# Kernel tuning notes

Hardware: AMD Instinct MI355X
Metric: run time of the kernel (lower is better)

Reference implementation:

```python
import jax, jax.numpy as jnp
import numpy as np

B, T, V, E, L, H = 128, 512, 128, 64, 128, 512  # batch, seq, vocab, char_emb, latent, hidden


def setup_inputs() -> dict:
    key = jax.random.key(0)
    ks = jax.random.split(key, 12)
    r = lambda k, shape, s=0.05: jax.random.normal(k, shape, dtype=jnp.float32) * s
    return {
        "char_ids": jax.random.randint(ks[0], (B, T), 0, V),
        "z": jax.random.normal(ks[1], (B, L), dtype=jnp.float32),
        "emb": r(ks[2], (V, E)),
        "cw1": r(ks[3], (L, H)), "cb1": jnp.zeros((H,)), "cg1": jnp.ones((H,)), "cbeta1": jnp.zeros((H,)),
        "cw2": r(ks[4], (H, H)), "cb2": jnp.zeros((H,)), "cg2": jnp.ones((H,)), "cbeta2": jnp.zeros((H,)),
        "wih0": r(ks[5], (4 * H, E + H + 2)), "whh0": r(ks[6], (4 * H, H)),
        "bih0": jnp.zeros((4 * H,)), "bhh0": jnp.zeros((4 * H,)),
        "wih1": r(ks[7], (4 * H, H)), "whh1": r(ks[8], (4 * H, H)),
        "bih1": jnp.zeros((4 * H,)), "bhh1": jnp.zeros((4 * H,)),
        "wo1": r(ks[9], (H, H // 2)), "bo1": jnp.zeros((H // 2,)),
        "wo2": r(ks[10], (H // 2, 2)), "bo2": jnp.zeros((2,)),
        "init_timing": jnp.zeros((2,)),
    }


def _ln(x, g, b, eps=1e-5):
    m = jnp.mean(x, -1, keepdims=True)
    v = jnp.var(x, -1, keepdims=True)
    return (x - m) * jax.lax.rsqrt(v + eps) * g + b


def _lstm_cell(x, h, c, wih, whh, bih, bhh):
    # PyTorch gate order: i, f, g, o
    gates = x @ wih.T + bih + h @ whh.T + bhh
    i, f, g, o = jnp.split(gates, 4, axis=-1)
    c = jax.nn.sigmoid(f) * c + jax.nn.sigmoid(i) * jnp.tanh(g)
    h = jax.nn.sigmoid(o) * jnp.tanh(c)
    return h, c


def reference(char_ids, z, emb, cw1, cb1, cg1, cbeta1, cw2, cb2, cg2, cbeta2,
              wih0, whh0, bih0, bhh0, wih1, whh1, bih1, bhh1,
              wo1, bo1, wo2, bo2, init_timing):
    b = char_ids.shape[0]
    # condition encoder: Linear -> LN -> LeakyReLU(0.2), twice
    cond = jax.nn.leaky_relu(_ln(z @ cw1 + cb1, cg1, cbeta1), 0.2)
    cond = jax.nn.leaky_relu(_ln(cond @ cw2 + cb2, cg2, cbeta2), 0.2)  # (B, H)
    xs = jnp.transpose(emb[char_ids], (1, 0, 2))  # (T, B, E)
    h0 = jnp.zeros((b, H), jnp.float32)
    c0 = jnp.zeros((b, H), jnp.float32)
    h1 = jnp.zeros((b, H), jnp.float32)
    c1 = jnp.zeros((b, H), jnp.float32)
    prev = jnp.broadcast_to(init_timing, (b, 2))

    def step(carry, xt):
        h0, c0, h1, c1, prev = carry
        xin = jnp.concatenate([xt, cond, prev], axis=-1)  # (B, E+H+2)
        h0, c0 = _lstm_cell(xin, h0, c0, wih0, whh0, bih0, bhh0)
        h1, c1 = _lstm_cell(h0, h1, c1, wih1, whh1, bih1, bhh1)
        out = jax.nn.leaky_relu(h1 @ wo1 + bo1, 0.2) @ wo2 + bo2
        out = jax.nn.softplus(out) + 0.005  # (B, 2)
        return (h0, c0, h1, c1, out), out

    _, ys = jax.lax.scan(step, (h0, c0, h1, c1, prev), xs)
    return jnp.transpose(ys, (1, 0, 2))  # (B, T, 2)
```

## Files before the change

kernel.cpp:

```cpp
#include <hip/hip_runtime.h>

#define Bn 128
#define Tn 512
#define Vn 128
#define En 64
#define Ln 128
#define Hn 512
#define G4 2048
#define WGS 256
#define NTHR 512
#define NALL (WGS * NTHR)
#define LSTR 520
#define GRPS 8
#define WPG 32
#define RPG 16

typedef unsigned short u16;
typedef unsigned int u32;
typedef __bf16 bf16x8 __attribute__((ext_vector_type(8)));
typedef float f32x4 __attribute__((ext_vector_type(4)));
typedef u32 u32x4 __attribute__((ext_vector_type(4)));

__device__ inline float bf2f(u16 h) {
    u32 u = ((u32)h) << 16;
    float f;
    __builtin_memcpy(&f, &u, 4);
    return f;
}
__device__ inline u16 f2bf(float f) {
    u32 u;
    __builtin_memcpy(&u, &f, 4);
    u32 r = (u + 0x7fffu + ((u >> 16) & 1u)) >> 16;
    return (u16)r;
}
__device__ inline u32 f2u(float f) { u32 u; __builtin_memcpy(&u, &f, 4); return u; }
__device__ inline float u2f(u32 u) { float f; __builtin_memcpy(&f, &u, 4); return f; }
__device__ inline float sigm(float x) { return 1.f / (1.f + expf(-x)); }
__device__ inline float leaky(float x) { return x > 0.f ? x : 0.2f * x; }
__device__ inline float softplus(float x) {
    return x > 0.f ? x + log1pf(expf(-x)) : log1pf(expf(x));
}

__device__ inline void cload16(const u32* p, u32* w) {
    u32x4 v0, v1, v2, v3;
    asm volatile(
        "global_load_dwordx4 %0, %4, off sc0 sc1\n\t"
        "global_load_dwordx4 %1, %4, off offset:16 sc0 sc1\n\t"
        "global_load_dwordx4 %2, %4, off offset:32 sc0 sc1\n\t"
        "global_load_dwordx4 %3, %4, off offset:48 sc0 sc1\n\t"
        "s_waitcnt vmcnt(0)"
        : "=&v"(v0), "=&v"(v1), "=&v"(v2), "=&v"(v3)
        : "v"(p)
        : "memory");
    *(u32x4*)(w) = v0;
    *(u32x4*)(w + 4) = v1;
    *(u32x4*)(w + 8) = v2;
    *(u32x4*)(w + 12) = v3;
}
__device__ inline u32 cload1(const u32* p) {
    u32 v;
    asm volatile("global_load_dword %0, %1, off sc0 sc1\n\ts_waitcnt vmcnt(0)"
                 : "=v"(v) : "v"(p) : "memory");
    return v;
}
__device__ inline void cwait() { asm volatile("s_waitcnt vmcnt(0)" ::: "memory"); }
__device__ inline void cstore1(u32* p, u32 v) {
    asm volatile("global_store_dword %0, %1, off sc0 sc1" :: "v"(p), "v"(v) : "memory");
}

#define OFF_FLAGS  0x000000
#define OFF_B1SUM  0x002000
#define OFF_WP     0x004000
#define OFF_BIAS0  0x008000
#define OFF_CPAR   0x00A000
#define OFF_H0P    0x010000
#define OFF_H1P    0x050000
#define OFF_PART   0x090000
#define OFF_WO1TH  0x0B0000
#define OFF_WO1TL  0x0F0000
#define OFF_ZF     0x130000
#define OFF_CW1F   0x140000
#define OFF_CW2F   0x180000
#define OFF_CONDF  0x280000
#define OFF_YBUF   0x2C0000
#define OFF_BASE0  0x300000
#define OFF_EMBW   0x400000
#define OFF_W0HI   0x500000
#define OFF_W0LO   0x700000
#define OFF_W1HI   0x900000
#define OFF_W1LO   0xB00000
#define OFF_WI1HI  0xD00000
#define OFF_WI1LO  0xF00000

__device__ inline void gbar_heavy(int* cnt, int* gen) {
    __syncthreads();
    if (threadIdx.x == 0) {
        __threadfence();
        int g = __hip_atomic_load(gen, __ATOMIC_RELAXED, __HIP_MEMORY_SCOPE_AGENT);
        int arrived = __hip_atomic_fetch_add(cnt, 1, __ATOMIC_ACQ_REL, __HIP_MEMORY_SCOPE_AGENT);
        if (arrived == WGS - 1) {
            __hip_atomic_store(cnt, 0, __ATOMIC_RELAXED, __HIP_MEMORY_SCOPE_AGENT);
            __hip_atomic_store(gen, g + 1, __ATOMIC_RELEASE, __HIP_MEMORY_SCOPE_AGENT);
        } else {
            while (__hip_atomic_load(gen, __ATOMIC_ACQUIRE, __HIP_MEMORY_SCOPE_AGENT) == g)
                __builtin_amdgcn_s_sleep(1);
        }
        __threadfence();
    }
    __syncthreads();
}

__device__ inline void poll32(const u32* gf, u32 sq) {
    const int l = threadIdx.x & 31;
    for (;;) {
        u32 v = cload1(gf + l);
        if (__all((int)(v >= sq))) break;
        __builtin_amdgcn_s_sleep(4);
    }
}
__device__ inline void poll16(const u32* gf, u32 sq) {
    const int l = threadIdx.x & 15;
    for (;;) {
        u32 v = cload1(gf + l);
        if (__all((int)(v >= sq))) break;
        __builtin_amdgcn_s_sleep(4);
    }
}

__device__ inline void unpack16(const u32* w, u16* ph, u16* pl) {
    u32 hd[8], ld[8];
#pragma unroll
    for (int i = 0; i < 8; ++i) {
        hd[i] = (w[2 * i] & 0xFFFFu) | (w[2 * i + 1] << 16);
        ld[i] = (w[2 * i] >> 16) | (w[2 * i + 1] & 0xFFFF0000u);
    }
    *(u32x4*)(ph) = *(const u32x4*)(hd);
    *(u32x4*)(ph + 8) = *(const u32x4*)(hd + 4);
    *(u32x4*)(pl) = *(const u32x4*)(ld);
    *(u32x4*)(pl + 8) = *(const u32x4*)(ld + 4);
}

#define MF(a, b, c) __builtin_amdgcn_mfma_f32_16x16x32_bf16(a, b, c, 0, 0, 0)

__device__ inline f32x4 gemm16_3(const u16* __restrict__ Ah, const u16* __restrict__ Al,
                                 const u16* __restrict__ Bhb, const u16* __restrict__ Blb,
                                 int colb, int n, int q) {
    const u16* Bh = Bhb + (size_t)(colb + n) * Hn;
    const u16* Bl = Blb + (size_t)(colb + n) * Hn;
    const int a0 = n * LSTR;
    f32x4 c0 = {0.f, 0.f, 0.f, 0.f}, c1 = c0, c2 = c0;
#pragma unroll 4
    for (int it = 0; it < 16; ++it) {
        const int ko = it * 32 + q * 8;
        bf16x8 bh = *(const bf16x8*)(Bh + ko);
        bf16x8 bl = *(const bf16x8*)(Bl + ko);
        bf16x8 ah = *(const bf16x8*)(Ah + a0 + ko);
        bf16x8 al = *(const bf16x8*)(Al + a0 + ko);
        c0 = MF(ah, bh, c0);
        c1 = MF(al, bh, c1);
        c2 = MF(ah, bl, c2);
    }
    return c0 + c1 + c2;
}

__device__ inline f32x4 gemm16_regB3(const u16* __restrict__ Ah, const u16* __restrict__ Al,
                                     const bf16x8* wa, const bf16x8* wb, int n, int q) {
    const int a0 = n * LSTR;
    f32x4 c0 = {0.f, 0.f, 0.f, 0.f}, c1 = c0, c2 = c0;
#pragma unroll
    for (int it = 0; it < 16; ++it) {
        const int ko = it * 32 + q * 8;
        bf16x8 ah = *(const bf16x8*)(Ah + a0 + ko);
        bf16x8 al = *(const bf16x8*)(Al + a0 + ko);
        c0 = MF(ah, wa[it], c0);
        c1 = MF(al, wa[it], c1);
        c2 = MF(ah, wb[it], c2);
    }
    return c0 + c1 + c2;
}

__device__ inline f32x4 gemm16_regB2(const u16* __restrict__ Ah, const u16* __restrict__ Al,
                                     const bf16x8* wb, int n, int q) {
    const int a0 = n * LSTR;
    f32x4 c0 = {0.f, 0.f, 0.f, 0.f}, c1 = c0;
#pragma unroll
    for (int it = 0; it < 16; ++it) {
        const int ko = it * 32 + q * 8;
        bf16x8 ah = *(const bf16x8*)(Ah + a0 + ko);
        bf16x8 al = *(const bf16x8*)(Al + a0 + ko);
        c0 = MF(ah, wb[it], c0);
        c1 = MF(al, wb[it], c1);
    }
    return c0 + c1;
}

__device__ inline f32x4 gemm16_ldsB3(const u16* __restrict__ Ah, const u16* __restrict__ Al,
                                     const u16* __restrict__ Bh, const u16* __restrict__ Bl,
                                     int n, int q) {
    const int a0 = n * LSTR;
    f32x4 c0 = {0.f, 0.f, 0.f, 0.f}, c1 = c0, c2 = c0;
#pragma unroll 4
    for (int it = 0; it < 16; ++it) {
        const int ko = it * 32 + q * 8;
        bf16x8 bh = *(const bf16x8*)(Bh + a0 + ko);
        bf16x8 bl = *(const bf16x8*)(Bl + a0 + ko);
        bf16x8 ah = *(const bf16x8*)(Ah + a0 + ko);
        bf16x8 al = *(const bf16x8*)(Al + a0 + ko);
        c0 = MF(ah, bh, c0);
        c1 = MF(al, bh, c1);
        c2 = MF(ah, bl, c2);
    }
    return c0 + c1 + c2;
}

__device__ inline void stage(float* dst, const void* src, int n, int gtid, bool isbf) {
    if (isbf) {
        const u16* s = (const u16*)src;
// ... 54 lines not shown
        e2 += ldw<ISBF>(emb, (size_t)(bb0 + 64) * En + k) * w;
        e3 += ldw<ISBF>(emb, (size_t)(bb0 + 96) * En + k) * w;
    }
    embW[(size_t)bb0 * G4 + cc] = e0;
    embW[(size_t)(bb0 + 32) * G4 + cc] = e1;
    embW[(size_t)(bb0 + 64) * G4 + cc] = e2;
    embW[(size_t)(bb0 + 96) * G4 + cc] = e3;
}

__device__ inline void ln_leaky_row(const float* __restrict__ x, const float* __restrict__ gamma,
                                    const float* __restrict__ beta, float* __restrict__ out,
                                    float* red) {
    int tid = threadIdx.x;
    float v = x[tid];
    float s = v, s2 = v * v;
    for (int off = 32; off; off >>= 1) {
        s += __shfl_down(s, off);
        s2 += __shfl_down(s2, off);
    }
    int wv = tid >> 6;
    if ((tid & 63) == 0) { red[wv * 2] = s; red[wv * 2 + 1] = s2; }
    __syncthreads();
    if (tid == 0) {
        float ts = 0.f, ts2 = 0.f;
        for (int i = 0; i < 8; ++i) { ts += red[i * 2]; ts2 += red[i * 2 + 1]; }
        float m = ts / 512.f;
        float var = ts2 / 512.f - m * m;
        red[16] = m;
        red[17] = rsqrtf(var + 1e-5f);
    }
    __syncthreads();
    float m = red[16], rs = red[17];
    out[tid] = leaky((v - m) * rs * gamma[tid] + beta[tid]);
    __syncthreads();
}

__global__ void init_flags_kernel(int* flags) { flags[threadIdx.x] = 0; }

__global__ __launch_bounds__(NTHR, 2) void gen_kernel(
    const int* __restrict__ char_ids, const void* z, const void* emb,
    const void* cw1, const void* cb1, const void* cg1, const void* cbeta1,
    const void* cw2, const void* cb2, const void* cg2, const void* cbeta2,
    const void* wih0, const void* whh0, const void* bih0, const void* bhh0,
    const void* wih1, const void* whh1, const void* bih1, const void* bhh1,
    const void* wo1, const void* bo1, const void* wo2, const void* bo2,
    const void* init_t, void* outp, char* __restrict__ ws) {
    __shared__ u16 lh0h[RPG * LSTR];
    __shared__ u16 lh0l[RPG * LSTR];
    __shared__ u16 lh1h[RPG * LSTR];
    __shared__ u16 lh1l[RPG * LSTR];
    __shared__ u16 lwoh[16 * LSTR];
    __shared__ u16 lwol[16 * LSTR];
    __shared__ float smemx[1024];
    __shared__ float pvs[32];
    __shared__ float red[34];

    int* flags = (int*)(ws + OFF_FLAGS);
    float* b1sum = (float*)(ws + OFF_B1SUM);
    float* wpb = (float*)(ws + OFF_WP);
    float* bias0f = (float*)(ws + OFF_BIAS0);
    float* cpar = (float*)(ws + OFF_CPAR);
    u32* h0p = (u32*)(ws + OFF_H0P);
    u32* h1p = (u32*)(ws + OFF_H1P);
    float* partf = (float*)(ws + OFF_PART);
    u16* wo1Th = (u16*)(ws + OFF_WO1TH);
    u16* wo1Tl = (u16*)(ws + OFF_WO1TL);
    float* zf = (float*)(ws + OFF_ZF);
    float* cw1f = (float*)(ws + OFF_CW1F);
    float* cw2f = (float*)(ws + OFF_CW2F);
    float* condf = (float*)(ws + OFF_CONDF);
    float* ybuf = (float*)(ws + OFF_YBUF);
    float* base0 = (float*)(ws + OFF_BASE0);
    float* embW = (float*)(ws + OFF_EMBW);
    u16* W0hi = (u16*)(ws + OFF_W0HI);
    u16* W0lo = (u16*)(ws + OFF_W0LO);
    u16* W1hi = (u16*)(ws + OFF_W1HI);
    u16* W1lo = (u16*)(ws + OFF_W1LO);
    u16* Wi1hi = (u16*)(ws + OFF_WI1HI);
    u16* Wi1lo = (u16*)(ws + OFF_WI1LO);
    float* wo1f = base0;

    const bool isbf = (((const u32*)cg1)[0] == 0x3F803F80u);

    const int g = blockIdx.x;
    const int tid = threadIdx.x;
    const int wv = tid >> 6;
    const int grp = g >> 5;
    const int ut = g & 31;
    const int mat = wv >> 2;
    const int gw = wv & 3;
    const int R0g = grp * RPG;
    const int colb = gw * 512 + ut * 16;
    const int lane = tid & 63;
    const int n = lane & 15;
    const int q = lane >> 4;
    const int gtid = g * NTHR + tid;
    const f32x4 Z4 = {0.f, 0.f, 0.f, 0.f};

    u32* gf = (u32*)flags + grp * 64;
    u32* gf2 = (u32*)flags + grp * 64 + 32;
    u32* gfl = gf + ut;
    int* hcnt = flags + 512;
    int* hgen = flags + 528;
    float* part = partf + grp * 1024;

    stage_split(W0hi, W0lo, whh0, G4 * Hn, gtid, isbf);
    stage_split(W1hi, W1lo, whh1, G4 * Hn, gtid, isbf);
    stage_split(Wi1hi, Wi1lo, wih1, G4 * Hn, gtid, isbf);
    stage(zf, z, Bn * Ln, gtid, isbf);
    stage(cw1f, cw1, Ln * Hn, gtid, isbf);
    stage(cw2f, cw2, Hn * Hn, gtid, isbf);
    stage(cpar + 0, cg1, 512, gtid, isbf);
    stage(cpar + 512, cbeta1, 512, gtid, isbf);
    stage(cpar + 1024, cg2, 512, gtid, isbf);
    stage(cpar + 1536, cbeta2, 512, gtid, isbf);
    stage(cpar + 2048, bo1, 256, gtid, isbf);
    stage(cpar + 2304, bo2, 2, gtid, isbf);
    stage(cpar + 2560, cb2, 512, gtid, isbf);
    stage(cpar + 3072, cb1, 512, gtid, isbf);
    stage(cpar + 3584, wo2, 256 * 2, gtid, isbf);
    stage(wo1f, wo1, Hn * 256, gtid, isbf);
    if (gtid < Bn * Hn) { cstore1(h0p + gtid, 0); cstore1(h1p + gtid, 0); }
    if (isbf) {
        if (gtid < G4) b1sum[gtid] = bf2f(((const u16*)bih1)[gtid]) + bf2f(((const u16*)bhh1)[gtid]);
        if (gtid < G4) bias0f[gtid] = bf2f(((const u16*)bih0)[gtid]) + bf2f(((const u16*)bhh0)[gtid]);
        if (gtid < 4096) {
            size_t ix = (size_t)(gtid >> 1) * 578 + 576 + (gtid & 1);
            wpb[gtid] = bf2f(((const u16*)wih0)[ix]);
        }
    } else {
        if (gtid < G4) b1sum[gtid] = ((const float*)bih1)[gtid] + ((const float*)bhh1)[gtid];
        if (gtid < G4) bias0f[gtid] = ((const float*)bih0)[gtid] + ((const float*)bhh0)[gtid];
        if (gtid < 4096) {
            size_t ix = (size_t)(gtid >> 1) * 578 + 576 + (gtid & 1);
            wpb[gtid] = ((const float*)wih0)[ix];
        }
    }
    gbar_heavy(hcnt, hgen);
    if (gtid < Bn * Hn) {
        int bb = gtid >> 9, nn = gtid & 511;
        float a = cpar[3072 + nn];
        const float* zr = zf + bb * Ln;
        for (int k = 0; k < Ln; ++k) a += zr[k] * cw1f[k * Hn + nn];
        ybuf[gtid] = a;
    }
    for (int e = gtid; e < 256 * Hn; e += NALL) {
        int nn = e >> 9, kk = e & 511;
        float w = wo1f[kk * 256 + nn];
        u16 hv = f2bf(w);
        wo1Th[e] = hv;
        wo1Tl[e] = f2bf(w - bf2f(hv));
    }
    gbar_heavy(hcnt, hgen);
    if (g < Bn) ln_leaky_row(ybuf + g * Hn, cpar + 0, cpar + 512, condf + g * Hn, red);
    gbar_heavy(hcnt, hgen);
    if (g < Bn) {
        float a = cpar[2560 + tid];
        const float* crow = condf + g * Hn;
        for (int k = 0; k < Hn; ++k) a += crow[k] * cw2f[k * Hn + tid];
        ybuf[g * Hn + tid] = a;
    }
    gbar_heavy(hcnt, hgen);
    if (g < Bn) ln_leaky_row(ybuf + g * Hn, cpar + 1024, cpar + 1536, condf + g * Hn, red);
    gbar_heavy(hcnt, hgen);
    if (gtid < Bn * Hn) {
        if (isbf) phase5<true>(wih0, emb, condf, bias0f, base0, embW, gtid);
        else phase5<false>(wih0, emb, condf, bias0f, base0, embW, gtid);
    }
    gbar_heavy(hcnt, hgen);

    const bool headwg = (ut < 16);
    bf16x8 wA[16], wB[16];
    {
        const u16* BhA = (mat == 0 ? W0hi : W1hi) + (size_t)(colb + n) * Hn;
        const u16* BhB;
        if (isbf) {
            if (mat == 1) BhB = Wi1hi + (size_t)(colb + n) * Hn;
            else if (headwg && wv == 0) BhB = wo1Th + (size_t)(ut * 16 + n) * Hn;
            else BhB = BhA;
        } else {
            BhB = (mat == 0 ? W0lo : W1lo) + (size_t)(colb + n) * Hn;
        }
#pragma unroll
        for (int it = 0; it < 16; ++it) {
            wA[it] = *(const bf16x8*)(BhA + it * 32 + q * 8);
            wB[it] = *(const bf16x8*)(BhB + it * 32 + q * 8);
        }
    }
    if (!isbf && headwg) {
        for (int e = tid; e < 16 * Hn; e += NTHR) {
            int col = e >> 9, k = e & 511;
            lwoh[col * LSTR + k] = wo1Th[(size_t)(ut * 16 + col) * Hn + k];
            lwol[col * LSTR + k] = wo1Tl[(size_t)(ut * 16 + col) * Hn + k];
        }
    }

    float c0 = 0.f, c1 = 0.f;
    const int lr = tid >> 4;
    const int un = tid & 15;
    const int bb = R0g + lr;
    const int uu = ut * 16 + un;
    const float* bo1f = cpar + 2048;
    const float* bo2f = cpar + 2304;
    const float* wo2f = cpar + 3584;
    const int srow = tid >> 5;
    const int blk = tid & 31;
    const int kub = blk * 16;
    f32x4 acc1c = Z4;

    for (int e = tid; e < RPG * LSTR; e += NTHR) {
        lh0h[e] = 0; lh0l[e] = 0; lh1h[e] = 0; lh1l[e] = 0;
    }
    if (tid < 32) pvs[tid] = isbf ? bf2f(((const u16*)init_t)[tid & 1])
                                  : ((const float*)init_t)[tid & 1];

    for (int t = 0; t < Tn; ++t) {
        if (t >= 1) {
            if (wv == 0) poll32(gf, 2 * (u32)t);
            __syncthreads();
            if (blk != ut) {
                u32 w[16];
                cload16(h1p + (size_t)(R0g + srow) * Hn + kub, w);
                unpack16(w, lh1h + srow * LSTR + kub, lh1l + srow * LSTR + kub);
            }
        }
        __syncthreads();
        if (headwg && wv == 0 && t >= 1) {
            f32x4 ha = isbf ? gemm16_regB2(lh1h, lh1l, wB, n, q)
                            : gemm16_ldsB3(lh1h, lh1l, lwoh, lwol, n, q);
            float p[4][2];
#pragma unroll
            for (int r = 0; r < 4; ++r) {
                float hv = leaky(ha[r] + bo1f[ut * 16 + n]);
                p[r][0] = hv * wo2f[(ut * 16 + n) * 2];
                p[r][1] = hv * wo2f[(ut * 16 + n) * 2 + 1];
            }
#pragma unroll
            for (int r = 0; r < 4; ++r)
#pragma unroll
                for (int j = 0; j < 2; ++j) {
                    float s = p[r][j];
                    s += __shfl_xor(s, 1, 16);
                    s += __shfl_xor(s, 2, 16);
                    s += __shfl_xor(s, 4, 16);
                    s += __shfl_xor(s, 8, 16);
                    p[r][j] = s;
                }
            if (n == 0) {
#pragma unroll
                for (int r = 0; r < 4; ++r)
#pragma unroll
                    for (int j = 0; j < 2; ++j) {
                        int row = q * 4 + r;
                        cstore1((u32*)(part + (row * 2 + j) * 16 + ut), f2u(p[r][j]));
                    }
            }
            cwait();
            if (tid == 0) cstore1(gf2 + ut, (u32)t);
        }
        if (mat == 0) {
            f32x4 a = isbf ? gemm16_regB2(lh0h, lh0l, wA, n, q)
                           : gemm16_regB3(lh0h, lh0l, wA, wB, n, q);
#pragma unroll
            for (int r = 0; r < 4; ++r)
                smemx[gw * 256 + (q * 4 + r) * 16 + n] = a[r];
        } else {
            acc1c = isbf ? gemm16_regB2(lh1h, lh1l, wA, n, q)
                         : gemm16_regB3(lh1h, lh1l, wA, wB, n, q);
        }
        if (t >= 1) {
            if (wv == 0) {
                poll16(gf2, (u32)t);
                if (tid < 32) {
                    int row = tid >> 1, j = tid & 1;
                    u32 hw[16];
                    cload16((const u32*)(part + (row * 2 + j) * 16), hw);
                    float s = bo2f[j];
#pragma unroll
                    for (int i = 0; i < 16; ++i) s += u2f(hw[i]);
                    float y = softplus(s) + 0.005f;
                    pvs[row * 2 + j] = y;
                    if (ut == 0) {
                        size_t oi = ((size_t)(R0g + row) * Tn + (t - 1)) * 2 + j;
                        if (isbf) ((u16*)outp)[oi] = f2bf(y);
                        else ((float*)outp)[oi] = y;
                    }
                }
            }
        }
        __syncthreads();
        if (tid < 256) {
            int id = char_ids[bb * Tn + t];
            float pv0 = pvs[lr * 2], pv1 = pvs[lr * 2 + 1];
            float gv[4];
#pragma unroll
            for (int gi = 0; gi < 4; ++gi) {
                int cc = gi * 512 + uu;
                gv[gi] = smemx[gi * 256 + lr * 16 + un] + base0[(size_t)bb * G4 + cc] +
                         embW[(size_t)id * G4 + cc] + pv0 * wpb[2 * cc] + pv1 * wpb[2 * cc + 1];
            }
            float ig = sigm(gv[0]), fg = sigm(gv[1]), gg = tanhf(gv[2]), og = sigm(gv[3]);
            c0 = fg * c0 + ig * gg;
            float h = og * tanhf(c0);
            u16 hv = f2bf(h);
            u16 lv = f2bf(h - bf2f(hv));
            lh0h[lr * LSTR + uu] = hv;
            lh0l[lr * LSTR + uu] = lv;
            cstore1(h0p + (size_t)bb * Hn + uu, (u32)hv | ((u32)lv << 16));
        }
        cwait();
        __syncthreads();
        if (tid == 0) cstore1(gfl, 2 * (u32)t + 1);

        if (wv == 0) poll32(gf, 2 * (u32)t + 1);
        __syncthreads();
        if (blk != ut) {
            u32 w[16];
            cload16(h0p + (size_t)(R0g + srow) * Hn + kub, w);
            unpack16(w, lh0h + srow * LSTR + kub, lh0l + srow * LSTR + kub);
        }
        __syncthreads();
        if (mat == 1) {
            f32x4 a = isbf ? gemm16_regB2(lh0h, lh0l, wB, n, q)
                           : gemm16_3(lh0h, lh0l, Wi1hi, Wi1lo, colb, n, q);
            acc1c = acc1c + a;
#pragma unroll
            for (int r = 0; r < 4; ++r)
                smemx[gw * 256 + (q * 4 + r) * 16 + n] = acc1c[r];
        }
        __syncthreads();
        if (tid < 256) {
            float gv[4];
#pragma unroll
            for (int gi = 0; gi < 4; ++gi) {
                int cc = gi * 512 + uu;
                gv[gi] = smemx[gi * 256 + lr * 16 + un] + b1sum[cc];
            }
            float ig = sigm(gv[0]), fg = sigm(gv[1]), gg = tanhf(gv[2]), og = sigm(gv[3]);
            c1 = fg * c1 + ig * gg;
            float h = og * tanhf(c1);
            u16 hv = f2bf(h);
            u16 lv = f2bf(h - bf2f(hv));
            lh1h[lr * LSTR + uu] = hv;
            lh1l[lr * LSTR + uu] = lv;
            cstore1(h1p + (size_t)bb * Hn + uu, (u32)hv | ((u32)lv << 16));
        }
        cwait();
        __syncthreads();
        if (tid == 0) cstore1(gfl, 2 * (u32)t + 2);
    }

    if (wv == 0) poll32(gf, 2 * (u32)Tn);
    __syncthreads();
    if (blk != ut) {
        u32 w[16];
        cload16(h1p + (size_t)(R0g + srow) * Hn + kub, w);
        unpack16(w, lh1h + srow * LSTR + kub, lh1l + srow * LSTR + kub);
    }
    __syncthreads();
    if (headwg && wv == 0) {
        f32x4 ha = isbf ? gemm16_regB2(lh1h, lh1l, wB, n, q)
                        : gemm16_ldsB3(lh1h, lh1l, lwoh, lwol, n, q);
        float p[4][2];
#pragma unroll
        for (int r = 0; r < 4; ++r) {
            float hv = leaky(ha[r] + bo1f[ut * 16 + n]);
            p[r][0] = hv * wo2f[(ut * 16 + n) * 2];
            p[r][1] = hv * wo2f[(ut * 16 + n) * 2 + 1];
        }
#pragma unroll
        for (int r = 0; r < 4; ++r)
#pragma unroll
            for (int j = 0; j < 2; ++j) {
                float s = p[r][j];
                s += __shfl_xor(s, 1, 16);
                s += __shfl_xor(s, 2, 16);
                s += __shfl_xor(s, 4, 16);
                s += __shfl_xor(s, 8, 16);
                p[r][j] = s;
            }
        if (n == 0) {
#pragma unroll
            for (int r = 0; r < 4; ++r)
#pragma unroll
                for (int j = 0; j < 2; ++j) {
                    int row = q * 4 + r;
                    cstore1((u32*)(part + (row * 2 + j) * 16 + ut), f2u(p[r][j]));
                }
        }
        cwait();
        if (tid == 0) cstore1(gf2 + ut, (u32)Tn);
    }
    if (ut == 0 && wv == 0) {
        poll16(gf2, (u32)Tn);
        if (tid < 32) {
            int row = tid >> 1, j = tid & 1;
            u32 hw[16];
            cload16((const u32*)(part + (row * 2 + j) * 16), hw);
            float s = bo2f[j];
#pragma unroll
            for (int i = 0; i < 16; ++i) s += u2f(hw[i]);
            float y = softplus(s) + 0.005f;
            size_t oi = ((size_t)(R0g + row) * Tn + (Tn - 1)) * 2 + j;
            if (isbf) ((u16*)outp)[oi] = f2bf(y);
            else ((float*)outp)[oi] = y;
        }
    }
}

extern "C" void kernel_launch(void* const* d_in, const int* in_sizes, int n_in,
                              void* d_out, int out_size, void* d_ws, size_t ws_size,
                              hipStream_t stream) {
    (void)in_sizes; (void)n_in; (void)out_size; (void)ws_size;
    init_flags_kernel<<<1, 1024, 0, stream>>>((int*)d_ws);
    gen_kernel<<<WGS, NTHR, 0, stream>>>(
        (const int*)d_in[0], d_in[1], d_in[2], d_in[3], d_in[4], d_in[5], d_in[6], d_in[7],
        d_in[8], d_in[9], d_in[10], d_in[11], d_in[12], d_in[13], d_in[14], d_in[15], d_in[16],
        d_in[17], d_in[18], d_in[19], d_in[20], d_in[21], d_in[22], d_in[23],
        d_out, (char*)d_ws);
}
```

Before: 8.736 ms.

## Compute output head redundantly per workgroup to drop cross-WG partial-sum sync

In the bf16 path, every workgroup now computes the full 256-wide output head itself. Each of its 8 waves handles 32 columns of wo1 held in registers, and the partial sums are reduced in shared memory. This removes the per-step global partial-sum stores, the poll on gf2 and the cross-workgroup reduction of the head output. The cost is redundant head matmuls in all workgroups, an extra 16-register weight array (wC), and streaming Wi1 from global memory each step instead of holding it in registers, which may raise memory traffic or register pressure.

```diff
diff --git a/kernel.cpp b/kernel.cpp
--- a/kernel.cpp
+++ b/kernel.cpp
@@ -163,6 +163,23 @@
     return c0 + c1 + c2;
 }
 
+__device__ inline f32x4 gemm16_s2(const u16* __restrict__ Ah, const u16* __restrict__ Al,
+                                  const u16* __restrict__ Bhb, int colb, int n, int q) {
+    const u16* Bh = Bhb + (size_t)(colb + n) * Hn;
+    const int a0 = n * LSTR;
+    f32x4 c0 = {0.f, 0.f, 0.f, 0.f}, c1 = c0;
+#pragma unroll 4
+    for (int it = 0; it < 16; ++it) {
+        const int ko = it * 32 + q * 8;
+        bf16x8 bh = *(const bf16x8*)(Bh + ko);
+        bf16x8 ah = *(const bf16x8*)(Ah + a0 + ko);
+        bf16x8 al = *(const bf16x8*)(Al + a0 + ko);
+        c0 = MF(ah, bh, c0);
+        c1 = MF(al, bh, c1);
+    }
+    return c0 + c1;
+}
+
 __device__ inline f32x4 gemm16_regB3(const u16* __restrict__ Ah, const u16* __restrict__ Al,
                                      const bf16x8* wa, const bf16x8* wb, int n, int q) {
     const int a0 = n * LSTR;
@@ -323,6 +340,7 @@
     __shared__ u16 lwoh[16 * LSTR];
     __shared__ u16 lwol[16 * LSTR];
     __shared__ float smemx[1024];
+    __shared__ float hpart[256];
     __shared__ float pvs[32];
     __shared__ float red[34];
 
@@ -441,21 +459,23 @@
     gbar_heavy(hcnt, hgen);
 
     const bool headwg = (ut < 16);
-    bf16x8 wA[16], wB[16];
+    bf16x8 wA[16], wB[16], wC[16];
     {
         const u16* BhA = (mat == 0 ? W0hi : W1hi) + (size_t)(colb + n) * Hn;
         const u16* BhB;
+        const u16* BhC;
         if (isbf) {
-            if (mat == 1) BhB = Wi1hi + (size_t)(colb + n) * Hn;
-            else if (headwg && wv == 0) BhB = wo1Th + (size_t)(ut * 16 + n) * Hn;
-            else BhB = BhA;
+            BhB = wo1Th + (size_t)(wv * 32 + n) * Hn;
+            BhC = wo1Th + (size_t)(wv * 32 + 16 + n) * Hn;
         } else {
             BhB = (mat == 0 ? W0lo : W1lo) + (size_t)(colb + n) * Hn;
+            BhC = BhA;
         }
 #pragma unroll
         for (int it = 0; it < 16; ++it) {
             wA[it] = *(const bf16x8*)(BhA + it * 32 + q * 8);
             wB[it] = *(const bf16x8*)(BhB + it * 32 + q * 8);
+            wC[it] = *(const bf16x8*)(BhC + it * 32 + q * 8);
         }
     }
     if (!isbf && headwg) {
@@ -477,6 +497,8 @@
     const int srow = tid >> 5;
     const int blk = tid & 31;
     const int kub = blk * 16;
+    const int hc0 = wv * 32 + n;
+    const int hc1 = hc0 + 16;
     f32x4 acc1c = Z4;
 
     for (int e = tid; e < RPG * LSTR; e += NTHR) {
@@ -496,9 +518,39 @@
             }
         }
         __syncthreads();
-        if (headwg && wv == 0 && t >= 1) {
-            f32x4 ha = isbf ? gemm16_regB2(lh1h, lh1l, wB, n, q)
-                            : gemm16_ldsB3(lh1h, lh1l, lwoh, lwol, n, q);
+        if (isbf) {
+            if (t >= 1) {
+                f32x4 hA = gemm16_regB2(lh1h, lh1l, wB, n, q);
+                f32x4 hB = gemm16_regB2(lh1h, lh1l, wC, n, q);
+                float p[4][2];
+#pragma unroll
+                for (int r = 0; r < 4; ++r) {
+                    float hva = leaky(hA[r] + bo1f[hc0]);
+                    float hvb = leaky(hB[r] + bo1f[hc1]);
+                    p[r][0] = hva * wo2f[hc0 * 2] + hvb * wo2f[hc1 * 2];
+                    p[r][1] = hva * wo2f[hc0 * 2 + 1] + hvb * wo2f[hc1 * 2 + 1];
+                }
+#pragma unroll
+                for (int r = 0; r < 4; ++r)
+#pragma unroll
+                    for (int j = 0; j < 2; ++j) {
+                        float s = p[r][j];
+                        s += __shfl_xor(s, 1, 16);
+                        s += __shfl_xor(s, 2, 16);
+                        s += __shfl_xor(s, 4, 16);
+                        s += __shfl_xor(s, 8, 16);
+                        p[r][j] = s;
+                    }
+                if (n == 0) {
+#pragma unroll
+                    for (int r = 0; r < 4; ++r) {
+                        hpart[wv * 32 + (q * 4 + r) * 2 + 0] = p[r][0];
+                        hpart[wv * 32 + (q * 4 + r) * 2 + 1] = p[r][1];
+                    }
+                }
+            }
+        } else if (headwg && wv == 0 && t >= 1) {
+            f32x4 ha = gemm16_ldsB3(lh1h, lh1l, lwoh, lwol, n, q);
             float p[4][2];
 #pragma unroll
             for (int r = 0; r < 4; ++r) {
@@ -539,27 +591,39 @@
             acc1c = isbf ? gemm16_regB2(lh1h, lh1l, wA, n, q)
                          : gemm16_regB3(lh1h, lh1l, wA, wB, n, q);
         }
-        if (t >= 1) {
-            if (wv == 0) {
-                poll16(gf2, (u32)t);
-                if (tid < 32) {
-                    int row = tid >> 1, j = tid & 1;
-                    u32 hw[16];
-                    cload16((const u32*)(part + (row * 2 + j) * 16), hw);
-                    float s = bo2f[j];
-#pragma unroll
-                    for (int i = 0; i < 16; ++i) s += u2f(hw[i]);
-                    float y = softplus(s) + 0.005f;
-                    pvs[row * 2 + j] = y;
-                    if (ut == 0) {
-                        size_t oi = ((size_t)(R0g + row) * Tn + (t - 1)) * 2 + j;
-                        if (isbf) ((u16*)outp)[oi] = f2bf(y);
-                        else ((float*)outp)[oi] = y;
-                    }
+        if (!isbf && t >= 1 && wv == 0) {
+            poll16(gf2, (u32)t);
+            if (tid < 32) {
+                int row = tid >> 1, j = tid & 1;
+                u32 hw[16];
+                cload16((const u32*)(part + (row * 2 + j) * 16), hw);
+                float s = bo2f[j];
+#pragma unroll
+                for (int i = 0; i < 16; ++i) s += u2f(hw[i]);
+                float y = softplus(s) + 0.005f;
+                pvs[row * 2 + j] = y;
+                if (ut == 0) {
+                    size_t oi = ((size_t)(R0g + row) * Tn + (t - 1)) * 2 + j;
+                    ((float*)outp)[oi] = y;
                 }
             }
         }
         __syncthreads();
+        if (isbf) {
+            if (t >= 1 && tid < 32) {
+                int row = tid >> 1, j = tid & 1;
+                float s = bo2f[j];
+#pragma unroll
+                for (int w8 = 0; w8 < 8; ++w8) s += hpart[w8 * 32 + row * 2 + j];
+                float y = softplus(s) + 0.005f;
+                pvs[row * 2 + j] = y;
+                if (ut == 0) {
+                    size_t oi = ((size_t)(R0g + row) * Tn + (t - 1)) * 2 + j;
+                    ((u16*)outp)[oi] = f2bf(y);
+                }
+            }
+            __syncthreads();
+        }
         if (tid < 256) {
             int id = char_ids[bb * Tn + t];
             float pv0 = pvs[lr * 2], pv1 = pvs[lr * 2 + 1];
@@ -592,7 +656,7 @@
         }
         __syncthreads();
         if (mat == 1) {
-            f32x4 a = isbf ? gemm16_regB2(lh0h, lh0l, wB, n, q)
+            f32x4 a = isbf ? gemm16_s2(lh0h, lh0l, Wi1hi, colb, n, q)
                            : gemm16_3(lh0h, lh0l, Wi1hi, Wi1lo, colb, n, q);
             acc1c = acc1c + a;
 #pragma unroll
@@ -621,60 +685,111 @@
         if (tid == 0) cstore1(gfl, 2 * (u32)t + 2);
     }
 
-    if (wv == 0) poll32(gf, 2 * (u32)Tn);
-    __syncthreads();
-    if (blk != ut) {
-        u32 w[16];
-        cload16(h1p + (size_t)(R0g + srow) * Hn + kub, w);
-        unpack16(w, lh1h + srow * LSTR + kub, lh1l + srow * LSTR + kub);
-    }
-    __syncthreads();
-    if (headwg && wv == 0) {
-        f32x4 ha = isbf ? gemm16_regB2(lh1h, lh1l, wB, n, q)
-                        : gemm16_ldsB3(lh1h, lh1l, lwoh, lwol, n, q);
-        float p[4][2];
-#pragma unroll
-        for (int r = 0; r < 4; ++r) {
-            float hv = leaky(ha[r] + bo1f[ut * 16 + n]);
-            p[r][0] = hv * wo2f[(ut * 16 + n) * 2];
-            p[r][1] = hv * wo2f[(ut * 16 + n) * 2 + 1];
-        }
-#pragma unroll
-        for (int r = 0; r < 4; ++r)
-#pragma unroll
-            for (int j = 0; j < 2; ++j) {
-                float s = p[r][j];
-                s += __shfl_xor(s, 1, 16);
-                s += __shfl_xor(s, 2, 16);
-                s += __shfl_xor(s, 4, 16);
-                s += __shfl_xor(s, 8, 16);
-                p[r][j] = s;
-            }
-        if (n == 0) {
+    if (isbf) {
+        if (ut == 0) {
+            if (wv == 0) poll32(gf, 2 * (u32)Tn);
+            __syncthreads();
+            if (blk != ut) {
+                u32 w[16];
+                cload16(h1p + (size_t)(R0g + srow) * Hn + kub, w);
+                unpack16(w, lh1h + srow * LSTR + kub, lh1l + srow * LSTR + kub);
+            }
+            __syncthreads();
+            {
+                f32x4 hA = gemm16_regB2(lh1h, lh1l, wB, n, q);
+                f32x4 hB = gemm16_regB2(lh1h, lh1l, wC, n, q);
+                float p[4][2];
+#pragma unroll
+                for (int r = 0; r < 4; ++r) {
+                    float hva = leaky(hA[r] + bo1f[hc0]);
+                    float hvb = leaky(hB[r] + bo1f[hc1]);
+                    p[r][0] = hva * wo2f[hc0 * 2] + hvb * wo2f[hc1 * 2];
+                    p[r][1] = hva * wo2f[hc0 * 2 + 1] + hvb * wo2f[hc1 * 2 + 1];
+                }
+#pragma unroll
+                for (int r = 0; r < 4; ++r)
+#pragma unroll
+                    for (int j = 0; j < 2; ++j) {
+                        float s = p[r][j];
+                        s += __shfl_xor(s, 1, 16);
+                        s += __shfl_xor(s, 2, 16);
+                        s += __shfl_xor(s, 4, 16);
+                        s += __shfl_xor(s, 8, 16);
+                        p[r][j] = s;
+                    }
+                if (n == 0) {
+#pragma unroll
+                    for (int r = 0; r < 4; ++r) {
+                        hpart[wv * 32 + (q * 4 + r) * 2 + 0] = p[r][0];
+                        hpart[wv * 32 + (q * 4 + r) * 2 + 1] = p[r][1];
+                    }
+                }
+            }
+            __syncthreads();
+            if (tid < 32) {
+                int row = tid >> 1, j = tid & 1;
+                float s = bo2f[j];
+#pragma unroll
+                for (int w8 = 0; w8 < 8; ++w8) s += hpart[w8 * 32 + row * 2 + j];
+                float y = softplus(s) + 0.005f;
+                size_t oi = ((size_t)(R0g + row) * Tn + (Tn - 1)) * 2 + j;
+                ((u16*)outp)[oi] = f2bf(y);
+            }
+        }
+    } else {
+        if (wv == 0) poll32(gf, 2 * (u32)Tn);
+        __syncthreads();
+        if (blk != ut) {
+            u32 w[16];
+            cload16(h1p + (size_t)(R0g + srow) * Hn + kub, w);
+            unpack16(w, lh1h + srow * LSTR + kub, lh1l + srow * LSTR + kub);
+        }
+        __syncthreads();
+        if (headwg && wv == 0) {
+            f32x4 ha = gemm16_ldsB3(lh1h, lh1l, lwoh, lwol, n, q);
+            float p[4][2];
+#pragma unroll
+            for (int r = 0; r < 4; ++r) {
+                float hv = leaky(ha[r] + bo1f[ut * 16 + n]);
+                p[r][0] = hv * wo2f[(ut * 16 + n) * 2];
+                p[r][1] = hv * wo2f[(ut * 16 + n) * 2 + 1];
+            }
 #pragma unroll
             for (int r = 0; r < 4; ++r)
 #pragma unroll
                 for (int j = 0; j < 2; ++j) {
-                    int row = q * 4 + r;
-                    cstore1((u32*)(part + (row * 2 + j) * 16 + ut), f2u(p[r][j]));
+                    float s = p[r][j];
+                    s += __shfl_xor(s, 1, 16);
+                    s += __shfl_xor(s, 2, 16);
+                    s += __shfl_xor(s, 4, 16);
+                    s += __shfl_xor(s, 8, 16);
+                    p[r][j] = s;
                 }
-        }
-        cwait();
-        if (tid == 0) cstore1(gf2 + ut, (u32)Tn);
-    }
-    if (ut == 0 && wv == 0) {
-        poll16(gf2, (u32)Tn);
-        if (tid < 32) {
-            int row = tid >> 1, j = tid & 1;
-            u32 hw[16];
-            cload16((const u32*)(part + (row * 2 + j) * 16), hw);
-            float s = bo2f[j];
-#pragma unroll
-            for (int i = 0; i < 16; ++i) s += u2f(hw[i]);
-            float y = softplus(s) + 0.005f;
-            size_t oi = ((size_t)(R0g + row) * Tn + (Tn - 1)) * 2 + j;
-            if (isbf) ((u16*)outp)[oi] = f2bf(y);
-            else ((float*)outp)[oi] = y;
+            if (n == 0) {
+#pragma unroll
+                for (int r = 0; r < 4; ++r)
+#pragma unroll
+                    for (int j = 0; j < 2; ++j) {
+                        int row = q * 4 + r;
+                        cstore1((u32*)(part + (row * 2 + j) * 16 + ut), f2u(p[r][j]));
+                    }
+            }
+            cwait();
+            if (tid == 0) cstore1(gf2 + ut, (u32)Tn);
+        }
+        if (ut == 0 && wv == 0) {
+            poll16(gf2, (u32)Tn);
+            if (tid < 32) {
+                int row = tid >> 1, j = tid & 1;
+                u32 hw[16];
+                cload16((const u32*)(part + (row * 2 + j) * 16), hw);
+                float s = bo2f[j];
+#pragma unroll
+                for (int i = 0; i < 16; ++i) s += u2f(hw[i]);
+                float y = softplus(s) + 0.005f;
+                size_t oi = ((size_t)(R0g + row) * Tn + (Tn - 1)) * 2 + j;
+                ((float*)outp)[oi] = y;
+            }
         }
     }
 }
```

Measured after the change: 14.49 ms. 65.8% more time.

## Tag partial sums with step epoch and reorder GEMM ahead of polling

Applied to the files above, without the earlier changes.

Each output-head partial is now stored together with its timestep tag as a dwordx2, and readers spin until all tags match. This replaces the separate flag-store, cwait and poll16 handshake. The layer-0 recurrent GEMM now starts at the top of each step, before the poll, so it can overlap the wait for other groups, and polling moves from wave 0 to wave 4. In the bf16 path, the layer-1 input GEMM now streams weights from global memory through a 2-MFMA routine instead of holding them in registers. This trades register pressure for extra global memory traffic.

```diff
diff --git a/kernel.cpp b/kernel.cpp
--- a/kernel.cpp
+++ b/kernel.cpp
@@ -20,6 +20,7 @@
 typedef __bf16 bf16x8 __attribute__((ext_vector_type(8)));
 typedef float f32x4 __attribute__((ext_vector_type(4)));
 typedef u32 u32x4 __attribute__((ext_vector_type(4)));
+typedef u32 u32x2 __attribute__((ext_vector_type(2)));
 
 __device__ inline float bf2f(u16 h) {
     u32 u = ((u32)h) << 16;
@@ -66,6 +67,41 @@
 __device__ inline void cwait() { asm volatile("s_waitcnt vmcnt(0)" ::: "memory"); }
 __device__ inline void cstore1(u32* p, u32 v) {
     asm volatile("global_store_dword %0, %1, off sc0 sc1" :: "v"(p), "v"(v) : "memory");
+}
+__device__ inline void cstore2(u32* p, u32 v, u32 e) {
+    u32x2 d;
+    d[0] = v;
+    d[1] = e;
+    asm volatile("global_store_dwordx2 %0, %1, off sc0 sc1" :: "v"(p), "v"(d) : "memory");
+}
+__device__ inline bool try16(const u32* p, u32 ep, u32* vals) {
+    u32x4 a0, a1, a2, a3, a4, a5, a6, a7;
+    asm volatile(
+        "global_load_dwordx4 %0, %8, off sc0 sc1\n\t"
+        "global_load_dwordx4 %1, %8, off offset:16 sc0 sc1\n\t"
+        "global_load_dwordx4 %2, %8, off offset:32 sc0 sc1\n\t"
+        "global_load_dwordx4 %3, %8, off offset:48 sc0 sc1\n\t"
+        "global_load_dwordx4 %4, %8, off offset:64 sc0 sc1\n\t"
+        "global_load_dwordx4 %5, %8, off offset:80 sc0 sc1\n\t"
+        "global_load_dwordx4 %6, %8, off offset:96 sc0 sc1\n\t"
+        "global_load_dwordx4 %7, %8, off offset:112 sc0 sc1\n\t"
+        "s_waitcnt vmcnt(0)"
+        : "=&v"(a0), "=&v"(a1), "=&v"(a2), "=&v"(a3),
+          "=&v"(a4), "=&v"(a5), "=&v"(a6), "=&v"(a7)
+        : "v"(p)
+        : "memory");
+    bool ok = (a0[1] == ep) & (a0[3] == ep) & (a1[1] == ep) & (a1[3] == ep) &
+              (a2[1] == ep) & (a2[3] == ep) & (a3[1] == ep) & (a3[3] == ep) &
+              (a4[1] == ep) & (a4[3] == ep) & (a5[1] == ep) & (a5[3] == ep) &
+              (a6[1] == ep) & (a6[3] == ep) & (a7[1] == ep) & (a7[3] == ep);
+    vals[0] = a0[0];  vals[1] = a0[2];  vals[2] = a1[0];  vals[3] = a1[2];
+    vals[4] = a2[0];  vals[5] = a2[2];  vals[6] = a3[0];  vals[7] = a3[2];
+    vals[8] = a4[0];  vals[9] = a4[2];  vals[10] = a5[0]; vals[11] = a5[2];
+    vals[12] = a6[0]; vals[13] = a6[2]; vals[14] = a7[0]; vals[15] = a7[2];
+    return ok;
+}
+__device__ inline void load16pairs(const u32* p, u32 ep, u32* vals) {
+    while (!try16(p, ep, vals)) __builtin_amdgcn_s_sleep(1);
 }
 
 #define OFF_FLAGS  0x000000
@@ -118,14 +154,6 @@
         __builtin_amdgcn_s_sleep(4);
     }
 }
-__device__ inline void poll16(const u32* gf, u32 sq) {
-    const int l = threadIdx.x & 15;
-    for (;;) {
-        u32 v = cload1(gf + l);
-        if (__all((int)(v >= sq))) break;
-        __builtin_amdgcn_s_sleep(4);
-    }
-}
 
 __device__ inline void unpack16(const u32* w, u16* ph, u16* pl) {
     u32 hd[8], ld[8];
@@ -163,6 +191,23 @@
     return c0 + c1 + c2;
 }
 
+__device__ inline f32x4 gemm16_s2(const u16* __restrict__ Ah, const u16* __restrict__ Al,
+                                  const u16* __restrict__ Bhb, int colb, int n, int q) {
+    const u16* Bh = Bhb + (size_t)(colb + n) * Hn;
+    const int a0 = n * LSTR;
+    f32x4 c0 = {0.f, 0.f, 0.f, 0.f}, c1 = c0;
+#pragma unroll 4
+    for (int it = 0; it < 16; ++it) {
+        const int ko = it * 32 + q * 8;
+        bf16x8 bh = *(const bf16x8*)(Bh + ko);
+        bf16x8 ah = *(const bf16x8*)(Ah + a0 + ko);
+        bf16x8 al = *(const bf16x8*)(Al + a0 + ko);
+        c0 = MF(ah, bh, c0);
+        c1 = MF(al, bh, c1);
+    }
+    return c0 + c1;
+}
+
 __device__ inline f32x4 gemm16_regB3(const u16* __restrict__ Ah, const u16* __restrict__ Al,
                                      const bf16x8* wa, const bf16x8* wb, int n, int q) {
     const int a0 = n * LSTR;
@@ -333,7 +378,7 @@
     float* cpar = (float*)(ws + OFF_CPAR);
     u32* h0p = (u32*)(ws + OFF_H0P);
     u32* h1p = (u32*)(ws + OFF_H1P);
-    float* partf = (float*)(ws + OFF_PART);
+    u32* partp = (u32*)(ws + OFF_PART);
     u16* wo1Th = (u16*)(ws + OFF_WO1TH);
     u16* wo1Tl = (u16*)(ws + OFF_WO1TL);
     float* zf = (float*)(ws + OFF_ZF);
@@ -369,11 +414,10 @@
     const f32x4 Z4 = {0.f, 0.f, 0.f, 0.f};
 
     u32* gf = (u32*)flags + grp * 64;
-    u32* gf2 = (u32*)flags + grp * 64 + 32;
     u32* gfl = gf + ut;
     int* hcnt = flags + 512;
     int* hgen = flags + 528;
-    float* part = partf + grp * 1024;
+    u32* ppart = partp + grp * 1024;
 
     stage_split(W0hi, W0lo, whh0, G4 * Hn, gtid, isbf);
     stage_split(W1hi, W1lo, whh1, G4 * Hn, gtid, isbf);
@@ -392,6 +436,7 @@
     stage(cpar + 3584, wo2, 256 * 2, gtid, isbf);
     stage(wo1f, wo1, Hn * 256, gtid, isbf);
     if (gtid < Bn * Hn) { cstore1(h0p + gtid, 0); cstore1(h1p + gtid, 0); }
+    if (gtid < 4096) cstore2(partp + (size_t)gtid * 2, 0u, 0u);
     if (isbf) {
         if (gtid < G4) b1sum[gtid] = bf2f(((const u16*)bih1)[gtid]) + bf2f(((const u16*)bhh1)[gtid]);
         if (gtid < G4) bias0f[gtid] = bf2f(((const u16*)bih0)[gtid]) + bf2f(((const u16*)bhh0)[gtid]);
@@ -486,8 +531,15 @@
                                   : ((const float*)init_t)[tid & 1];
 
     for (int t = 0; t < Tn; ++t) {
+        if (mat == 0) {
+            f32x4 a = isbf ? gemm16_regB2(lh0h, lh0l, wA, n, q)
+                           : gemm16_regB3(lh0h, lh0l, wA, wB, n, q);
+#pragma unroll
+            for (int r = 0; r < 4; ++r)
+                smemx[gw * 256 + (q * 4 + r) * 16 + n] = a[r];
+        }
         if (t >= 1) {
-            if (wv == 0) poll32(gf, 2 * (u32)t);
+            if (wv == 4) poll32(gf, 2 * (u32)t);
             __syncthreads();
             if (blk != ut) {
                 u32 w[16];
@@ -523,40 +575,28 @@
 #pragma unroll
                     for (int j = 0; j < 2; ++j) {
                         int row = q * 4 + r;
-                        cstore1((u32*)(part + (row * 2 + j) * 16 + ut), f2u(p[r][j]));
+                        cstore2(ppart + ((size_t)(row * 2 + j) * 16 + ut) * 2,
+                                f2u(p[r][j]), (u32)t);
                     }
             }
-            cwait();
-            if (tid == 0) cstore1(gf2 + ut, (u32)t);
-        }
-        if (mat == 0) {
-            f32x4 a = isbf ? gemm16_regB2(lh0h, lh0l, wA, n, q)
-                           : gemm16_regB3(lh0h, lh0l, wA, wB, n, q);
-#pragma unroll
-            for (int r = 0; r < 4; ++r)
-                smemx[gw * 256 + (q * 4 + r) * 16 + n] = a[r];
-        } else {
+        }
+        if (mat == 1) {
             acc1c = isbf ? gemm16_regB2(lh1h, lh1l, wA, n, q)
                          : gemm16_regB3(lh1h, lh1l, wA, wB, n, q);
         }
-        if (t >= 1) {
-            if (wv == 0) {
-                poll16(gf2, (u32)t);
-                if (tid < 32) {
-                    int row = tid >> 1, j = tid & 1;
-                    u32 hw[16];
-                    cload16((const u32*)(part + (row * 2 + j) * 16), hw);
-                    float s = bo2f[j];
-#pragma unroll
-                    for (int i = 0; i < 16; ++i) s += u2f(hw[i]);
-                    float y = softplus(s) + 0.005f;
-                    pvs[row * 2 + j] = y;
-                    if (ut == 0) {
-                        size_t oi = ((size_t)(R0g + row) * Tn + (t - 1)) * 2 + j;
-                        if (isbf) ((u16*)outp)[oi] = f2bf(y);
-                        else ((float*)outp)[oi] = y;
-                    }
-                }
+        if (t >= 1 && wv == 0 && tid < 32) {
+            int row = tid >> 1, j = tid & 1;
+            u32 hw[16];
+            load16pairs(ppart + ((size_t)(row * 2 + j) * 16) * 2, (u32)t, hw);
+            float s = bo2f[j];
+#pragma unroll
+            for (int i = 0; i < 16; ++i) s += u2f(hw[i]);
+            float y = softplus(s) + 0.005f;
+            pvs[row * 2 + j] = y;
+            if (ut == 0) {
+                size_t oi = ((size_t)(R0g + row) * Tn + (t - 1)) * 2 + j;
+                if (isbf) ((u16*)outp)[oi] = f2bf(y);
+                else ((float*)outp)[oi] = y;
             }
         }
         __syncthreads();
@@ -592,7 +632,7 @@
         }
         __syncthreads();
         if (mat == 1) {
-            f32x4 a = isbf ? gemm16_regB2(lh0h, lh0l, wB, n, q)
+            f32x4 a = isbf ? gemm16_s2(lh0h, lh0l, Wi1hi, colb, n, q)
                            : gemm16_3(lh0h, lh0l, Wi1hi, Wi1lo, colb, n, q);
             acc1c = acc1c + a;
 #pragma unroll
@@ -656,26 +696,22 @@
 #pragma unroll
                 for (int j = 0; j < 2; ++j) {
                     int row = q * 4 + r;
-                    cstore1((u32*)(part + (row * 2 + j) * 16 + ut), f2u(p[r][j]));
+                    cstore2(ppart + ((size_t)(row * 2 + j) * 16 + ut) * 2,
+                            f2u(p[r][j]), (u32)Tn);
                 }
         }
-        cwait();
-        if (tid == 0) cstore1(gf2 + ut, (u32)Tn);
-    }
-    if (ut == 0 && wv == 0) {
-        poll16(gf2, (u32)Tn);
-        if (tid < 32) {
-            int row = tid >> 1, j = tid & 1;
-            u32 hw[16];
-            cload16((const u32*)(part + (row * 2 + j) * 16), hw);
-            float s = bo2f[j];
-#pragma unroll
-            for (int i = 0; i < 16; ++i) s += u2f(hw[i]);
-            float y = softplus(s) + 0.005f;
-            size_t oi = ((size_t)(R0g + row) * Tn + (Tn - 1)) * 2 + j;
-            if (isbf) ((u16*)outp)[oi] = f2bf(y);
-            else ((float*)outp)[oi] = y;
-        }
+    }
+    if (ut == 0 && tid < 32) {
+        int row = tid >> 1, j = tid & 1;
+        u32 hw[16];
+        load16pairs(ppart + ((size_t)(row * 2 + j) * 16) * 2, (u32)Tn, hw);
+        float s = bo2f[j];
+#pragma unroll
+        for (int i = 0; i < 16; ++i) s += u2f(hw[i]);
+        float y = softplus(s) + 0.005f;
+        size_t oi = ((size_t)(R0g + row) * Tn + (Tn - 1)) * 2 + j;
+        if (isbf) ((u16*)outp)[oi] = f2bf(y);
+        else ((float*)outp)[oi] = y;
     }
 }
 
```

Measured after the change: 10.42 ms. 1.19x slower.

## Replace per-step head partial-sum flags with fixed-point 64-bit atomic accumulators

Applied to the files above, without the earlier changes.

Each of the 16 head workgroups now adds its output-head partial into a per-timestep 64-bit slot using a fixed-point atomicAdd. A count packed in the upper 16 bits lets consumers poll that single slot, replacing the separate partial buffer, the flag store and the 16-flag poll followed by a gather. This aims to remove one store-flag-poll round trip from the serial recurrence. In bf16 mode the layer-1 input GEMM also drops the low-weight product and reads weights from global instead of registers, which trades some precision and adds memory traffic. Fixed-point quantisation at 2^-24 and the accumulator range could affect accuracy.

```diff
diff --git a/kernel.cpp b/kernel.cpp
--- a/kernel.cpp
+++ b/kernel.cpp
@@ -17,9 +17,11 @@
 
 typedef unsigned short u16;
 typedef unsigned int u32;
+typedef unsigned long long u64;
 typedef __bf16 bf16x8 __attribute__((ext_vector_type(8)));
 typedef float f32x4 __attribute__((ext_vector_type(4)));
 typedef u32 u32x4 __attribute__((ext_vector_type(4)));
+typedef u32 u32x2 __attribute__((ext_vector_type(2)));
 
 __device__ inline float bf2f(u16 h) {
     u32 u = ((u32)h) << 16;
@@ -63,6 +65,12 @@
                  : "=v"(v) : "v"(p) : "memory");
     return v;
 }
+__device__ inline u64 cload2(const u64* p) {
+    u32x2 v;
+    asm volatile("global_load_dwordx2 %0, %1, off sc0 sc1\n\ts_waitcnt vmcnt(0)"
+                 : "=v"(v) : "v"(p) : "memory");
+    return ((u64)v[1] << 32) | (u64)v[0];
+}
 __device__ inline void cwait() { asm volatile("s_waitcnt vmcnt(0)" ::: "memory"); }
 __device__ inline void cstore1(u32* p, u32 v) {
     asm volatile("global_store_dword %0, %1, off sc0 sc1" :: "v"(p), "v"(v) : "memory");
@@ -75,10 +83,10 @@
 #define OFF_CPAR   0x00A000
 #define OFF_H0P    0x010000
 #define OFF_H1P    0x050000
-#define OFF_PART   0x090000
 #define OFF_WO1TH  0x0B0000
 #define OFF_WO1TL  0x0F0000
 #define OFF_ZF     0x130000
+#define OFF_PACC   0x130000
 #define OFF_CW1F   0x140000
 #define OFF_CW2F   0x180000
 #define OFF_CONDF  0x280000
@@ -92,6 +100,9 @@
 #define OFF_WI1HI  0xD00000
 #define OFF_WI1LO  0xF00000
 
+#define PSCALE 16777216.0f
+#define PINV   5.9604644775390625e-8f
+
 __device__ inline void gbar_heavy(int* cnt, int* gen) {
     __syncthreads();
     if (threadIdx.x == 0) {
@@ -112,14 +123,6 @@
 
 __device__ inline void poll32(const u32* gf, u32 sq) {
     const int l = threadIdx.x & 31;
-    for (;;) {
-        u32 v = cload1(gf + l);
-        if (__all((int)(v >= sq))) break;
-        __builtin_amdgcn_s_sleep(4);
-    }
-}
-__device__ inline void poll16(const u32* gf, u32 sq) {
-    const int l = threadIdx.x & 15;
     for (;;) {
         u32 v = cload1(gf + l);
         if (__all((int)(v >= sq))) break;
@@ -163,6 +166,23 @@
     return c0 + c1 + c2;
 }
 
+__device__ inline f32x4 gemm16_s2(const u16* __restrict__ Ah, const u16* __restrict__ Al,
+                                  const u16* __restrict__ Bhb, int colb, int n, int q) {
+    const u16* Bh = Bhb + (size_t)(colb + n) * Hn;
+    const int a0 = n * LSTR;
+    f32x4 c0 = {0.f, 0.f, 0.f, 0.f}, c1 = c0;
+#pragma unroll 4
+    for (int it = 0; it < 16; ++it) {
+        const int ko = it * 32 + q * 8;
+        bf16x8 bh = *(const bf16x8*)(Bh + ko);
+        bf16x8 ah = *(const bf16x8*)(Ah + a0 + ko);
+        bf16x8 al = *(const bf16x8*)(Al + a0 + ko);
+        c0 = MF(ah, bh, c0);
+        c1 = MF(al, bh, c1);
+    }
+    return c0 + c1;
+}
+
 __device__ inline f32x4 gemm16_regB3(const u16* __restrict__ Ah, const u16* __restrict__ Al,
                                      const bf16x8* wa, const bf16x8* wb, int n, int q) {
     const int a0 = n * LSTR;
@@ -333,7 +353,7 @@
     float* cpar = (float*)(ws + OFF_CPAR);
     u32* h0p = (u32*)(ws + OFF_H0P);
     u32* h1p = (u32*)(ws + OFF_H1P);
-    float* partf = (float*)(ws + OFF_PART);
+    u64* paccb = (u64*)(ws + OFF_PACC);
     u16* wo1Th = (u16*)(ws + OFF_WO1TH);
     u16* wo1Tl = (u16*)(ws + OFF_WO1TL);
     float* zf = (float*)(ws + OFF_ZF);
@@ -369,11 +389,10 @@
     const f32x4 Z4 = {0.f, 0.f, 0.f, 0.f};
 
     u32* gf = (u32*)flags + grp * 64;
-    u32* gf2 = (u32*)flags + grp * 64 + 32;
     u32* gfl = gf + ut;
     int* hcnt = flags + 512;
     int* hgen = flags + 528;
-    float* part = partf + grp * 1024;
+    u64* pacc = paccb + (size_t)grp * Tn * 32;
 
     stage_split(W0hi, W0lo, whh0, G4 * Hn, gtid, isbf);
     stage_split(W1hi, W1lo, whh1, G4 * Hn, gtid, isbf);
@@ -438,6 +457,10 @@
         if (isbf) phase5<true>(wih0, emb, condf, bias0f, base0, embW, gtid);
         else phase5<false>(wih0, emb, condf, bias0f, base0, embW, gtid);
     }
+    for (int e = gtid; e < GRPS * Tn * 32; e += NALL) {
+        cstore1((u32*)paccb + 2 * e, 0);
+        cstore1((u32*)paccb + 2 * e + 1, 0);
+    }
     gbar_heavy(hcnt, hgen);
 
     const bool headwg = (ut < 16);
@@ -518,16 +541,17 @@
                     p[r][j] = s;
                 }
             if (n == 0) {
+                u64* acc = pacc + (size_t)(t - 1) * 32;
 #pragma unroll
                 for (int r = 0; r < 4; ++r)
 #pragma unroll
                     for (int j = 0; j < 2; ++j) {
                         int row = q * 4 + r;
-                        cstore1((u32*)(part + (row * 2 + j) * 16 + ut), f2u(p[r][j]));
+                        long long fx = (long long)llrintf(p[r][j] * PSCALE);
+                        u64 x = (1ULL << 48) + (u64)(fx + (1LL << 40));
+                        atomicAdd(acc + (row * 2 + j), x);
                     }
             }
-            cwait();
-            if (tid == 0) cstore1(gf2 + ut, (u32)t);
         }
         if (mat == 0) {
             f32x4 a = isbf ? gemm16_regB2(lh0h, lh0l, wA, n, q)
@@ -539,24 +563,24 @@
             acc1c = isbf ? gemm16_regB2(lh1h, lh1l, wA, n, q)
                          : gemm16_regB3(lh1h, lh1l, wA, wB, n, q);
         }
-        if (t >= 1) {
-            if (wv == 0) {
-                poll16(gf2, (u32)t);
-                if (tid < 32) {
-                    int row = tid >> 1, j = tid & 1;
-                    u32 hw[16];
-                    cload16((const u32*)(part + (row * 2 + j) * 16), hw);
-                    float s = bo2f[j];
-#pragma unroll
-                    for (int i = 0; i < 16; ++i) s += u2f(hw[i]);
-                    float y = softplus(s) + 0.005f;
-                    pvs[row * 2 + j] = y;
-                    if (ut == 0) {
-                        size_t oi = ((size_t)(R0g + row) * Tn + (t - 1)) * 2 + j;
-                        if (isbf) ((u16*)outp)[oi] = f2bf(y);
-                        else ((float*)outp)[oi] = y;
-                    }
-                }
+        if (t >= 1 && wv == 0 && tid < 32) {
+            int row = tid >> 1, j = tid & 1;
+            u64* slot = pacc + (size_t)(t - 1) * 32 + tid;
+            u64 v;
+            for (;;) {
+                v = cload2(slot);
+                if ((v >> 48) == 16) break;
+                __builtin_amdgcn_s_sleep(2);
+            }
+            v = cload2(slot);
+            long long fx = (long long)(v & 0xFFFFFFFFFFFFULL) - (16LL << 40);
+            float s = bo2f[j] + (float)fx * PINV;
+            float y = softplus(s) + 0.005f;
+            pvs[row * 2 + j] = y;
+            if (ut == 0) {
+                size_t oi = ((size_t)(R0g + row) * Tn + (t - 1)) * 2 + j;
+                if (isbf) ((u16*)outp)[oi] = f2bf(y);
+                else ((float*)outp)[oi] = y;
             }
         }
         __syncthreads();
@@ -592,7 +616,7 @@
         }
         __syncthreads();
         if (mat == 1) {
-            f32x4 a = isbf ? gemm16_regB2(lh0h, lh0l, wB, n, q)
+            f32x4 a = isbf ? gemm16_s2(lh0h, lh0l, Wi1hi, colb, n, q)
                            : gemm16_3(lh0h, lh0l, Wi1hi, Wi1lo, colb, n, q);
             acc1c = acc1c + a;
 #pragma unroll
@@ -651,31 +675,34 @@
                 p[r][j] = s;
             }
         if (n == 0) {
+            u64* acc = pacc + (size_t)(Tn - 1) * 32;
 #pragma unroll
             for (int r = 0; r < 4; ++r)
 #pragma unroll
                 for (int j = 0; j < 2; ++j) {
                     int row = q * 4 + r;
-                    cstore1((u32*)(part + (row * 2 + j) * 16 + ut), f2u(p[r][j]));
+                    long long fx = (long long)llrintf(p[r][j] * PSCALE);
+                    u64 x = (1ULL << 48) + (u64)(fx + (1LL << 40));
+                    atomicAdd(acc + (row * 2 + j), x);
                 }
         }
-        cwait();
-        if (tid == 0) cstore1(gf2 + ut, (u32)Tn);
-    }
-    if (ut == 0 && wv == 0) {
-        poll16(gf2, (u32)Tn);
-        if (tid < 32) {
-            int row = tid >> 1, j = tid & 1;
-            u32 hw[16];
-            cload16((const u32*)(part + (row * 2 + j) * 16), hw);
-            float s = bo2f[j];
-#pragma unroll
-            for (int i = 0; i < 16; ++i) s += u2f(hw[i]);
-            float y = softplus(s) + 0.005f;
-            size_t oi = ((size_t)(R0g + row) * Tn + (Tn - 1)) * 2 + j;
-            if (isbf) ((u16*)outp)[oi] = f2bf(y);
-            else ((float*)outp)[oi] = y;
-        }
+    }
+    if (ut == 0 && wv == 0 && tid < 32) {
+        int row = tid >> 1, j = tid & 1;
+        u64* slot = pacc + (size_t)(Tn - 1) * 32 + tid;
+        u64 v;
+        for (;;) {
+            v = cload2(slot);
+            if ((v >> 48) == 16) break;
+            __builtin_amdgcn_s_sleep(2);
+        }
+        v = cload2(slot);
+        long long fx = (long long)(v & 0xFFFFFFFFFFFFULL) - (16LL << 40);
+        float s = bo2f[j] + (float)fx * PINV;
+        float y = softplus(s) + 0.005f;
+        size_t oi = ((size_t)(R0g + row) * Tn + (Tn - 1)) * 2 + j;
+        if (isbf) ((u16*)outp)[oi] = f2bf(y);
+        else ((float*)outp)[oi] = y;
     }
 }
 
```

New measurement: 13.76 ms. 1.57x slower.
